# Kernel tuning notes

Measured on AMD Instinct MI355X. Metric: run time of the kernel, lower is better.

## Reference

```python
import jax, jax.numpy as jnp
import numpy as np

S_CONST = float(np.log(9.0))   # self.s = log(9)
K = 1.0                        # soft_sign sharpness (config.k)
RHO = 1.0
ALPHA0 = 0.01
BETA0 = 0.1
DECAY = 0.99


def soft_sign(x, k=K):
    # E2Efold soft sign: sigmoid(2*k*x)
    return jax.nn.sigmoid(2.0 * k * x)


def constraint_matrix(x):
    # x: [B, L, 4] -> m: [B, L, L]; pairing constraint AU+CG+UG outer products,
    # symmetrized, with |i-j|<=3 band zeroed (diags mask in torch version).
    base_a, base_u, base_c, base_g = x[..., 0], x[..., 1], x[..., 2], x[..., 3]

    def sym_outer(p, q):
        m = p[:, :, None] * q[:, None, :]
        return m + jnp.swapaxes(m, -1, -2)

    m = sym_outer(base_a, base_u) + sym_outer(base_c, base_g) + sym_outer(base_u, base_g)
    L = x.shape[1]
    i = jnp.arange(L)
    band = jnp.abs(i[:, None] - i[None, :]) <= 3  # [L, L] bool
    return jnp.where(band, jnp.zeros((), m.dtype), m)


def contact_a(a_hat, m):
    a = a_hat * a_hat
    a = (a + jnp.swapaxes(a, -1, -2)) * 0.5
    return a * m


def setup_inputs() -> dict:
    key = jax.random.key(0)
    k1, k2 = jax.random.split(key)
    B, L = 16, 512
    u = jax.random.normal(k1, (B, L, L), jnp.float32) * 2.0
    x = jax.random.uniform(k2, (B, L, 4), jnp.float32)
    return {"u": u, "x": x, "timesteps": 20}


def reference(u, x, timesteps):
    m = constraint_matrix(x)
    u = soft_sign(u - S_CONST) * u
    a_hat = jax.nn.sigmoid(u) * jax.lax.stop_gradient(soft_sign(u - S_CONST))
    a = contact_a(a_hat, m)
    lmbd = jax.lax.stop_gradient(jax.nn.relu(jnp.sum(a, -1) - 1.0))

    # per-step decayed learning rates: step t uses alpha0*decay^t (for grad step)
    # and alpha0*decay^(t+1) for the soft-threshold (torch decays alpha in between)
    t_idx = jnp.arange(timesteps, dtype=jnp.float32)
    alphas = ALPHA0 * DECAY ** t_idx
    betas = BETA0 * DECAY ** t_idx

    def step(carry, ab):
        lmbd, a, a_hat = carry
        alpha, beta = ab
        grad_a = -u / 2.0 + (lmbd * soft_sign(jnp.sum(a, -1) - 1.0))[..., None]
        grad = a_hat * m * (grad_a + jnp.swapaxes(grad_a, -1, -2))
        a_hat_new = a_hat - alpha * grad
        a_hat_new = jax.nn.relu(jnp.abs(a_hat_new) - RHO * alpha * DECAY)
        a_hat_new = jnp.clip(a_hat_new, -1.0, 1.0)
        a_new = contact_a(a_hat_new, m)
        lmbd_new = lmbd + beta * jax.nn.relu(jnp.sum(a_new, -1) - 1.0)
        return (lmbd_new, a_new, a_hat_new), a_new

    _, a_stack = jax.lax.scan(step, (lmbd, a, a_hat), (alphas, betas))
    return a_stack  # [timesteps, B, L, L] == a_t_list[1:]
```

## Files before the change

kernel.cpp:

```cpp
#include <hip/hip_runtime.h>
#include <math.h>

#define BB 16
#define LL 512
#define TS 20
#define TT 64
#define NT (LL / TT)
#define NPAIR (NT * (NT + 1) / 2)
#define NUNIT 32
#define NBLK (BB * NUNIT)
#define BLL (BB * LL * LL)
#define NROW (BB * LL)
#define RSPSTEP (BB * NT * LL)

#define S_CONST 2.19722457733621938f

typedef float float4n __attribute__((ext_vector_type(4)));

__device__ __forceinline__ float sgm(float v) { return 1.0f / (1.0f + __expf(-v)); }
__device__ __forceinline__ float ahat_of(float up) {
  return sgm(up) * sgm(2.0f * (up - S_CONST));
}

__device__ __forceinline__ void st_agent(float* p, float v) {
  __hip_atomic_store(p, v, __ATOMIC_RELAXED, __HIP_MEMORY_SCOPE_AGENT);
}
__device__ __forceinline__ float ld_agent(const float* p) {
  return __hip_atomic_load(p, __ATOMIC_RELAXED, __HIP_MEMORY_SCOPE_AGENT);
}

__device__ __forceinline__ void bar_lds() {
  asm volatile("s_waitcnt lgkmcnt(0)" ::: "memory");
  __builtin_amdgcn_s_barrier();
  asm volatile("" ::: "memory");
}

__device__ __forceinline__ void decode_unit(int p, int& RI, int& RJ, bool& dg) {
  if (p < 28) {
    int base = 0, i = 0;
    while (p >= base + (NT - 1 - i)) { base += NT - 1 - i; ++i; }
    RI = i;
    RJ = i + 1 + (p - base);
    dg = false;
  } else {
    int g = p - 28;
    RI = 2 * g;
    RJ = 2 * g + 1;
    dg = true;
  }
}

__global__ __launch_bounds__(256, 2) void k_fused(const float* __restrict__ u,
                                                  const float* __restrict__ x,
                                                  float* __restrict__ rsp,
                                                  float* __restrict__ out) {
  __shared__ float t1[TT][TT + 1];
  __shared__ float t2[TT][TT + 1];
  __shared__ float colp1[16][TT];
  __shared__ float colp2[16][TT];
  __shared__ float rp1[TT];
  __shared__ float rp2[TT];
  __shared__ float xr[2][TT][4];
  __shared__ float xt[2][TT][4];
  __shared__ float cI[TT];
  __shared__ float cJ[TT];

  int b = blockIdx.x / NUNIT;
  int p = blockIdx.x % NUNIT;
  int RI, RJ;
  bool dg;
  decode_unit(p, RI, RJ, dg);
  int C1 = dg ? RI : RJ;
  int C2 = dg ? RJ : RI;

  int tid = threadIdx.x;
  int tx = tid & 15, ty = tid >> 4;

  if (tid < 128) {
    int which = tid >> 6;
    int r = tid & 63;
    int gi = (which ? RJ : RI) * TT + r;
    const float* xp = x + ((b * LL) + gi) * 4;
    float A = xp[0], U = xp[1], C = xp[2], G = xp[3];
    xr[which][r][0] = A; xr[which][r][1] = U; xr[which][r][2] = C; xr[which][r][3] = G;
    xt[which][r][0] = U; xt[which][r][1] = A + G; xt[which][r][2] = G; xt[which][r][3] = C + U;
  }

  int lrow = 0;
  if (tid < 128) {
    int which = tid >> 6;
    int r = tid & 63;
    lrow = (which ? RJ : RI) * TT + r;
  }
  float lmbd = 0.0f;

  float av1[4][4], av2[4][4];
  float wv1[4][4], wv2[4][4];
  float mv1[4][4], mv2[4][4];

  __syncthreads();

#pragma unroll
  for (int k = 0; k < 4; ++k) {
    int r = ty + 16 * k;
    {
      int i = RI * TT + r;
      int off = (b * LL + i) * LL + C1 * TT + 4 * tx;
      float4 u4 = *reinterpret_cast<const float4*>(u + off);
      float uu[4] = {u4.x, u4.y, u4.z, u4.w};
#pragma unroll
      for (int q = 0; q < 4; ++q) {
        float up = sgm(2.0f * (uu[q] - S_CONST)) * uu[q];
        t1[r][4 * tx + q] = up;
        av1[k][q] = ahat_of(up);
      }
    }
    {
      int i = RJ * TT + r;
      int off = (b * LL + i) * LL + C2 * TT + 4 * tx;
      float4 u4 = *reinterpret_cast<const float4*>(u + off);
      float uu[4] = {u4.x, u4.y, u4.z, u4.w};
#pragma unroll
      for (int q = 0; q < 4; ++q) {
        float up = sgm(2.0f * (uu[q] - S_CONST)) * uu[q];
        t2[r][4 * tx + q] = up;
        av2[k][q] = ahat_of(up);
      }
    }
  }
  __syncthreads();

  {
    float (*T1)[TT + 1] = dg ? t1 : t2;
    float (*T2)[TT + 1] = dg ? t2 : t1;
    float (*xc1)[4] = dg ? xt[0] : xt[1];
    float (*xc2)[4] = dg ? xt[1] : xt[0];
    float* rsp0 = rsp;

#pragma unroll
    for (int k = 0; k < 4; ++k) {
      int r = ty + 16 * k;
      {
        int i = RI * TT + r;
        float rs = 0.0f;
#pragma unroll
        for (int q = 0; q < 4; ++q) {
          int c = 4 * tx + q;
          int j = C1 * TT + c;
          float upT = T1[c][r];
          wv1[k][q] = -(t1[r][c] + upT);
          int d = i - j; d = d < 0 ? -d : d;
          float mm = (d <= 3) ? 0.0f
                              : xr[0][r][0] * xc1[c][0] + xr[0][r][1] * xc1[c][1] +
                                    xr[0][r][2] * xc1[c][2] + xr[0][r][3] * xc1[c][3];
          float mh = 0.5f * mm;
          mv1[k][q] = mh;
          float aT = ahat_of(upT);
          float a = av1[k][q];
          rs += (a * a + aT * aT) * mh;
        }
        rs += __shfl_xor(rs, 1); rs += __shfl_xor(rs, 2);
        rs += __shfl_xor(rs, 4); rs += __shfl_xor(rs, 8);
        if (tx == 0) st_agent(&rsp0[(b * NT + C1) * LL + i], rs + 1.0f);
      }
      {
        int i = RJ * TT + r;
        float rs = 0.0f;
#pragma unroll
        for (int q = 0; q < 4; ++q) {
          int c = 4 * tx + q;
          int j = C2 * TT + c;
          float upT = T2[c][r];
          wv2[k][q] = -(t2[r][c] + upT);
          int d = i - j; d = d < 0 ? -d : d;
          float mm = (d <= 3) ? 0.0f
                              : xr[1][r][0] * xc2[c][0] + xr[1][r][1] * xc2[c][1] +
                                    xr[1][r][2] * xc2[c][2] + xr[1][r][3] * xc2[c][3];
          float mh = 0.5f * mm;
          mv2[k][q] = mh;
          float aT = ahat_of(upT);
          float a = av2[k][q];
          rs += (a * a + aT * aT) * mh;
        }
        rs += __shfl_xor(rs, 1); rs += __shfl_xor(rs, 2);
        rs += __shfl_xor(rs, 4); rs += __shfl_xor(rs, 8);
        if (tx == 0) st_agent(&rsp0[(b * NT + C2) * LL + i], rs + 1.0f);
      }
    }
  }

  float (*T1)[TT + 1] = dg ? t1 : t2;
  float (*T2)[TT + 1] = dg ? t2 : t1;

  float alpha = 0.01f;
  float beta_prev = 0.0f;

  for (int t = 0; t < TS; ++t) {
    if (tid < 128) {
      const float* rp = rsp + (size_t)t * RSPSTEP + b * NT * LL + lrow;
      float v0, v1, v2, v3, v4, v5, v6, v7;
      for (;;) {
        v0 = ld_agent(rp + 0 * LL);
        v1 = ld_agent(rp + 1 * LL);
        v2 = ld_agent(rp + 2 * LL);
        v3 = ld_agent(rp + 3 * LL);
        v4 = ld_agent(rp + 4 * LL);
        v5 = ld_agent(rp + 5 * LL);
        v6 = ld_agent(rp + 6 * LL);
        v7 = ld_agent(rp + 7 * LL);
        bool ok = (v0 != 0.0f) & (v1 != 0.0f) & (v2 != 0.0f) & (v3 != 0.0f) &
                  (v4 != 0.0f) & (v5 != 0.0f) & (v6 != 0.0f) & (v7 != 0.0f);
        if (__all(ok)) break;
        __builtin_amdgcn_s_sleep(2);
        asm volatile("" ::: "memory");
      }
      float rsv = ((v0 + v1) + (v2 + v3)) + ((v4 + v5) + (v6 + v7));
      float dv = rsv - 9.0f;
      float rel = dv > 0.0f ? dv : 0.0f;
      lmbd = (t == 0) ? rel : lmbd + beta_prev * rel;
      float cv2 = 2.0f * (lmbd * sgm(2.0f * dv));
      if (tid >= 64) cJ[tid & 63] = cv2; else cI[tid] = cv2;
    }
    bar_lds();

    float thr = alpha * 0.99f;
    float* cc1 = dg ? cI : cJ;
    float* cc2 = dg ? cJ : cI;

    float cq1[4], cq2[4];
#pragma unroll
    for (int q = 0; q < 4; ++q) {
      cq1[q] = cc1[4 * tx + q];
      cq2[q] = cc2[4 * tx + q];
    }

    float cp1[4] = {0.f, 0.f, 0.f, 0.f};
    float cp2[4] = {0.f, 0.f, 0.f, 0.f};
#pragma unroll
    for (int k = 0; k < 4; ++k) {
      int r = ty + 16 * k;
      {
        float ci = cI[r];
        float rsv = 0.0f;
#pragma unroll
        for (int q = 0; q < 4; ++q) {
          int c = 4 * tx + q;
          float a = av1[k][q];
          float mh = mv1[k][q];
          float s2 = wv1[k][q] + ci + cq1[q];
          float tt = mh * s2;
          float sc = fmaf(-alpha, tt, 1.0f);
          float an = a * sc;
          float f = fabsf(an) - thr;
          an = fminf(fmaxf(f, 0.0f), 1.0f);
          av1[k][q] = an;
          float v = an * an * mh;
          t1[r][c] = v;
          rsv += v;
          cp1[q] += v;
        }
        rsv += __shfl_xor(rsv, 1); rsv += __shfl_xor(rsv, 2);
        rsv += __shfl_xor(rsv, 4); rsv += __shfl_xor(rsv, 8);
        if (tx == 0) rp1[r] = rsv;
      }
      {
        float ci = cJ[r];
        float rsv = 0.0f;
#pragma unroll
        for (int q = 0; q < 4; ++q) {
          int c = 4 * tx + q;
          float a = av2[k][q];
          float mh = mv2[k][q];
          float s2 = wv2[k][q] + ci + cq2[q];
          float tt = mh * s2;
          float sc = fmaf(-alpha, tt, 1.0f);
          float an = a * sc;
          float f = fabsf(an) - thr;
          an = fminf(fmaxf(f, 0.0f), 1.0f);
          av2[k][q] = an;
          float v = an * an * mh;
          t2[r][c] = v;
          rsv += v;
          cp2[q] += v;
        }
        rsv += __shfl_xor(rsv, 1); rsv += __shfl_xor(rsv, 2);
        rsv += __shfl_xor(rsv, 4); rsv += __shfl_xor(rsv, 8);
        if (tx == 0) rp2[r] = rsv;
      }
    }
#pragma unroll
    for (int q = 0; q < 4; ++q) {
      colp1[ty][4 * tx + q] = cp1[q];
      colp2[ty][4 * tx + q] = cp2[q];
    }
    bar_lds();

    if (tid < 128) {
      if (t < TS - 1) {
        float* rs_next = rsp + (size_t)(t + 1) * RSPSTEP;
        if (tid < 64) {
          int i = tid;
          float vsum = rp1[i];
          float (*cpA)[TT] = dg ? colp1 : colp2;
#pragma unroll
          for (int y = 0; y < 16; ++y) vsum += cpA[y][i];
          st_agent(&rs_next[(b * NT + C1) * LL + RI * TT + i], vsum + 1.0f);
        } else {
          int i = tid - 64;
          float vsum = rp2[i];
          float (*cpB)[TT] = dg ? colp2 : colp1;
#pragma unroll
          for (int y = 0; y < 16; ++y) vsum += cpB[y][i];
          st_agent(&rs_next[(b * NT + C2) * LL + RJ * TT + i], vsum + 1.0f);
        }
      }
    } else {
      int tid2 = tid - 128;
      int tx2 = tid2 & 15, ty2 = tid2 >> 4;
      float* op = out + (size_t)t * BLL;
#pragma unroll
      for (int k = 0; k < 8; ++k) {
        int r = ty2 + 8 * k;
        {
          int off = (b * LL + RI * TT + r) * LL + C1 * TT + 4 * tx2;
          float4n res;
#pragma unroll
          for (int q = 0; q < 4; ++q) {
            int c = 4 * tx2 + q;
            res[q] = t1[r][c] + T1[c][r];
          }
          __builtin_nontemporal_store(res, reinterpret_cast<float4n*>(op + off));
        }
        {
          int off = (b * LL + RJ * TT + r) * LL + C2 * TT + 4 * tx2;
          float4n res;
#pragma unroll
          for (int q = 0; q < 4; ++q) {
            int c = 4 * tx2 + q;
            res[q] = t2[r][c] + T2[c][r];
          }
          __builtin_nontemporal_store(res, reinterpret_cast<float4n*>(op + off));
        }
      }
    }

    beta_prev = (t == 0) ? 0.1f : beta_prev * 0.99f;
    alpha *= 0.99f;
  }
}

__device__ __forceinline__ void decode_pair(int p, int& I, int& J) {
  int base = 0, i = 0;
  while (p >= base + (NT - i)) { base += NT - i; ++i; }
  I = i;
  J = i + (p - base);
}

__global__ __launch_bounds__(256) void k_init(const float* __restrict__ u,
                                              const float* __restrict__ x,
                                              float* __restrict__ w,
                                              float* __restrict__ ah,
                                              float* __restrict__ rowsum) {
  __shared__ float up1[TT][TT + 1];
  __shared__ float up2[TT][TT + 1];
  __shared__ float xr[2][TT][4];
  __shared__ float xt[2][TT][4];

  int b = blockIdx.x / NPAIR;
  int p = blockIdx.x % NPAIR;
  int I, J;
  decode_pair(p, I, J);
  bool diag = (I == J);
  int tid = threadIdx.x;
  int tx = tid & 15, ty = tid >> 4;

  if (tid < 128) {
    int which = tid >> 6;
    int r = tid & 63;
    int gi = (which ? J : I) * TT + r;
    const float* xp = x + ((b * LL) + gi) * 4;
    float A = xp[0], U = xp[1], C = xp[2], G = xp[3];
    xr[which][r][0] = A; xr[which][r][1] = U; xr[which][r][2] = C; xr[which][r][3] = G;
    xt[which][r][0] = U; xt[which][r][1] = A + G; xt[which][r][2] = G; xt[which][r][3] = C + U;
  }

  float a1r[4][4], a2r[4][4];

#pragma unroll
  for (int k = 0; k < 4; ++k) {
    int r = ty + 16 * k;
    {
      int i = I * TT + r;
      int off = (b * LL + i) * LL + J * TT + 4 * tx;
      float4 u4 = *reinterpret_cast<const float4*>(u + off);
      float uu[4] = {u4.x, u4.y, u4.z, u4.w};
      float av[4];
#pragma unroll
      for (int q = 0; q < 4; ++q) {
        float up = sgm(2.0f * (uu[q] - S_CONST)) * uu[q];
        up1[r][4 * tx + q] = up;
        av[q] = ahat_of(up);
        a1r[k][q] = av[q];
      }
      *reinterpret_cast<float4*>(ah + off) = make_float4(av[0], av[1], av[2], av[3]);
    }
    if (!diag) {
      int i = J * TT + r;
      int off = (b * LL + i) * LL + I * TT + 4 * tx;
      float4 u4 = *reinterpret_cast<const float4*>(u + off);
      float uu[4] = {u4.x, u4.y, u4.z, u4.w};
      float av[4];
#pragma unroll
      for (int q = 0; q < 4; ++q) {
        float up = sgm(2.0f * (uu[q] - S_CONST)) * uu[q];
        up2[r][4 * tx + q] = up;
        av[q] = ahat_of(up);
        a2r[k][q] = av[q];
      }
      *reinterpret_cast<float4*>(ah + off) = make_float4(av[0], av[1], av[2], av[3]);
    }
  }
  __syncthreads();

  float (*U2)[TT + 1] = diag ? up1 : up2;

#pragma unroll
  for (int k = 0; k < 4; ++k) {
    int r = ty + 16 * k;
    {
      int i = I * TT + r;
      int off = (b * LL + i) * LL + J * TT + 4 * tx;
      float wv[4];
      float rs = 0.0f;
#pragma unroll
      for (int q = 0; q < 4; ++q) {
        int c = 4 * tx + q;
        int j = J * TT + c;
        float upT = U2[c][r];
        wv[q] = -0.5f * (up1[r][c] + upT);
        int d = i - j; d = d < 0 ? -d : d;
        float mm = (d <= 3) ? 0.0f
                            : xr[0][r][0] * xt[1][c][0] + xr[0][r][1] * xt[1][c][1] +
                                  xr[0][r][2] * xt[1][c][2] + xr[0][r][3] * xt[1][c][3];
        float aT = ahat_of(upT);
        float a = a1r[k][q];
        rs += 0.5f * (a * a + aT * aT) * mm;
      }
      *reinterpret_cast<float4*>(w + off) = make_float4(wv[0], wv[1], wv[2], wv[3]);
      rs += __shfl_xor(rs, 1); rs += __shfl_xor(rs, 2);
      rs += __shfl_xor(rs, 4); rs += __shfl_xor(rs, 8);
      if (tx == 0) atomicAdd(&rowsum[b * LL + i], rs);
    }
    if (!diag) {
      int i = J * TT + r;
      int off = (b * LL + i) * LL + I * TT + 4 * tx;
      float wv[4];
      float rs = 0.0f;
#pragma unroll
      for (int q = 0; q < 4; ++q) {
        int c = 4 * tx + q;
        int j = I * TT + c;
        float upT = up1[c][r];
        wv[q] = -0.5f * (up2[r][c] + upT);
        int d = i - j; d = d < 0 ? -d : d;
        float mm = (d <= 3) ? 0.0f
                            : xr[1][r][0] * xt[0][c][0] + xr[1][r][1] * xt[0][c][1] +
                                  xr[1][r][2] * xt[0][c][2] + xr[1][r][3] * xt[0][c][3];
        float aT = ahat_of(upT);
        float a = a2r[k][q];
        rs += 0.5f * (a * a + aT * aT) * mm;
      }
      *reinterpret_cast<float4*>(w + off) = make_float4(wv[0], wv[1], wv[2], wv[3]);
      rs += __shfl_xor(rs, 1); rs += __shfl_xor(rs, 2);
      rs += __shfl_xor(rs, 4); rs += __shfl_xor(rs, 8);
      if (tx == 0) atomicAdd(&rowsum[b * LL + i], rs);
    }
  }
}

__global__ __launch_bounds__(256) void k_c(float* __restrict__ lmbd,
                                           const float* __restrict__ rs,
                                           float* __restrict__ cc,
                                           float* __restrict__ rsn,
                                           float beta_prev, int first) {
  int idx = blockIdx.x * blockDim.x + threadIdx.x;
  if (idx >= NROW) return;
  float t = rs[idx] - 1.0f;
  float rel = t > 0.0f ? t : 0.0f;
  float l = first ? rel : lmbd[idx] + beta_prev * rel;
  lmbd[idx] = l;
  cc[idx] = l * sgm(2.0f * t);
  rsn[idx] = 0.0f;
}

__global__ __launch_bounds__(256) void k_step(const float* __restrict__ x,
                                              const float* __restrict__ w,
                                              float* __restrict__ ah,
                                              const float* __restrict__ cvec,
                                              float* __restrict__ rsn,
                                              float* __restrict__ out,
                                              float alpha, float thr) {
  __shared__ float an1[TT][TT + 1];
  __shared__ float an2[TT][TT + 1];
  __shared__ float xr[2][TT][4];
  __shared__ float xt[2][TT][4];
  __shared__ float cI[TT];
  __shared__ float cJ[TT];

  int b = blockIdx.x / NPAIR;
  int p = blockIdx.x % NPAIR;
  int I, J;
  decode_pair(p, I, J);
  bool diag = (I == J);
  int tid = threadIdx.x;
  int tx = tid & 15, ty = tid >> 4;

  if (tid < 128) {
    int which = tid >> 6;
    int r = tid & 63;
    int gi = (which ? J : I) * TT + r;
    const float* xp = x + ((b * LL) + gi) * 4;
    float A = xp[0], U = xp[1], C = xp[2], G = xp[3];
    xr[which][r][0] = A; xr[which][r][1] = U; xr[which][r][2] = C; xr[which][r][3] = G;
    xt[which][r][0] = U; xt[which][r][1] = A + G; xt[which][r][2] = G; xt[which][r][3] = C + U;
  } else {
    int t2i = tid - 128;
    int which = t2i >> 6;
    int r = t2i & 63;
    int gi = (which ? J : I) * TT + r;
    float cv = cvec[b * LL + gi];
    if (which) cJ[r] = cv; else cI[r] = cv;
  }
  __syncthreads();

  float m1[4][4], m2[4][4];

#pragma unroll
  for (int k = 0; k < 4; ++k) {
    int r = ty + 16 * k;
    {
      int i = I * TT + r;
      int off = (b * LL + i) * LL + J * TT + 4 * tx;
      float4 a4 = *reinterpret_cast<const float4*>(ah + off);
      float4 w4 = *reinterpret_cast<const float4*>(w + off);
      float av[4] = {a4.x, a4.y, a4.z, a4.w};
      float wv[4] = {w4.x, w4.y, w4.z, w4.w};
      float ci = cI[r];
      float res[4];
#pragma unroll
      for (int q = 0; q < 4; ++q) {
        int c = 4 * tx + q;
        int j = J * TT + c;
        int d = i - j; d = d < 0 ? -d : d;
        float mm = (d <= 3) ? 0.0f
                            : xr[0][r][0] * xt[1][c][0] + xr[0][r][1] * xt[1][c][1] +
                                  xr[0][r][2] * xt[1][c][2] + xr[0][r][3] * xt[1][c][3];
        m1[k][q] = mm;
        float g = av[q] * mm * (wv[q] + ci + cJ[c]);
        float an = av[q] - alpha * g;
        an = fabsf(an) - thr;
        an = an > 0.0f ? an : 0.0f;
        an = an < 1.0f ? an : 1.0f;
        res[q] = an;
        an1[r][c] = an;
      }
      *reinterpret_cast<float4*>(ah + off) = make_float4(res[0], res[1], res[2], res[3]);
    }
    if (!diag) {
      int i = J * TT + r;
      int off = (b * LL + i) * LL + I * TT + 4 * tx;
      float4 a4 = *reinterpret_cast<const float4*>(ah + off);
      float4 w4 = *reinterpret_cast<const float4*>(w + off);
      float av[4] = {a4.x, a4.y, a4.z, a4.w};
      float wv[4] = {w4.x, w4.y, w4.z, w4.w};
      float ci = cJ[r];
      float res[4];
#pragma unroll
      for (int q = 0; q < 4; ++q) {
        int c = 4 * tx + q;
        int j = I * TT + c;
        int d = i - j; d = d < 0 ? -d : d;
        float mm = (d <= 3) ? 0.0f
                            : xr[1][r][0] * xt[0][c][0] + xr[1][r][1] * xt[0][c][1] +
                                  xr[1][r][2] * xt[0][c][2] + xr[1][r][3] * xt[0][c][3];
        m2[k][q] = mm;
        float g = av[q] * mm * (wv[q] + ci + cI[c]);
        float an = av[q] - alpha * g;
        an = fabsf(an) - thr;
        an = an > 0.0f ? an : 0.0f;
        an = an < 1.0f ? an : 1.0f;
        res[q] = an;
        an2[r][c] = an;
      }
      *reinterpret_cast<float4*>(ah + off) = make_float4(res[0], res[1], res[2], res[3]);
    }
  }
  __syncthreads();

  float (*A2)[TT + 1] = diag ? an1 : an2;

#pragma unroll
  for (int k = 0; k < 4; ++k) {
    int r = ty + 16 * k;
    {
      int i = I * TT + r;
      int off = (b * LL + i) * LL + J * TT + 4 * tx;
      float res[4];
      float rs = 0.0f;
#pragma unroll
      for (int q = 0; q < 4; ++q) {
        int c = 4 * tx + q;
        float a = an1[r][c];
        float bt = A2[c][r];
        float v = 0.5f * (a * a + bt * bt) * m1[k][q];
        res[q] = v;
        rs += v;
      }
      *reinterpret_cast<float4*>(out + off) = make_float4(res[0], res[1], res[2], res[3]);
      rs += __shfl_xor(rs, 1); rs += __shfl_xor(rs, 2);
      rs += __shfl_xor(rs, 4); rs += __shfl_xor(rs, 8);
      if (tx == 0) atomicAdd(&rsn[b * LL + i], rs);
    }
    if (!diag) {
      int i = J * TT + r;
      int off = (b * LL + i) * LL + I * TT + 4 * tx;
      float res[4];
      float rs = 0.0f;
#pragma unroll
      for (int q = 0; q < 4; ++q) {
        int c = 4 * tx + q;
        float a = an2[r][c];
        float bt = an1[c][r];
        float v = 0.5f * (a * a + bt * bt) * m2[k][q];
        res[q] = v;
        rs += v;
      }
      *reinterpret_cast<float4*>(out + off) = make_float4(res[0], res[1], res[2], res[3]);
      rs += __shfl_xor(rs, 1); rs += __shfl_xor(rs, 2);
      rs += __shfl_xor(rs, 4); rs += __shfl_xor(rs, 8);
      if (tx == 0) atomicAdd(&rsn[b * LL + i], rs);
    }
  }
}

extern "C" void kernel_launch(void* const* d_in, const int* in_sizes, int n_in,
                              void* d_out, int out_size, void* d_ws, size_t ws_size,
                              hipStream_t stream) {
  const float* u = (const float*)d_in[0];
  const float* x = (const float*)d_in[1];
  float* out = (float*)d_out;
  float* ws = (float*)d_ws;

  float* rsp = ws;
  (void)hipMemsetAsync(rsp, 0, (size_t)TS * RSPSTEP * sizeof(float), stream);

  void* args[] = {(void*)&u, (void*)&x, (void*)&rsp, (void*)&out};
  hipError_t err = hipLaunchCooperativeKernel((void*)k_fused, dim3(NBLK),
                                              dim3(256), args, 0, stream);
  if (err == hipSuccess) return;

  float* w = ws;
  float* ah = ws + (size_t)BLL;
  float* rsA = ws + 2 * (size_t)BLL;
  float* rsB = rsA + NROW;
  float* cc = rsB + NROW;
  float* lmbd = cc + NROW;

  (void)hipMemsetAsync(rsA, 0, NROW * sizeof(float), stream);

  dim3 grid(BB * NPAIR);
  dim3 block(256);
  k_init<<<grid, block, 0, stream>>>(u, x, w, ah, rsA);

  float* ra = rsA;
  float* rb = rsB;
  for (int t = 0; t < TS; ++t) {
    float alpha = 0.01f * powf(0.99f, (float)t);
    float beta_prev = (t > 0) ? 0.1f * powf(0.99f, (float)(t - 1)) : 0.0f;
    k_c<<<dim3((NROW + 255) / 256), block, 0, stream>>>(lmbd, ra, cc, rb, beta_prev,
                                                        t == 0 ? 1 : 0);
    k_step<<<grid, block, 0, stream>>>(x, w, ah, cc, rb, out + (size_t)t * BLL, alpha,
                                       alpha * 0.99f);
    float* tmp = ra; ra = rb; rb = tmp;
  }
}
```

Measured before the change: 398.6 us.

## Add row-panel cooperative kernel holding full rows and transpose in registers

```diff
diff --git a/kernel.cpp b/kernel.cpp
--- a/kernel.cpp
+++ b/kernel.cpp
@@ -4,6 +4,18 @@
 #define BB 16
 #define LL 512
 #define TS 20
+
+#define NPANEL 16
+#define PROWS 32
+#define NBLK2 (BB * NPANEL)
+#define CROWS (BB * LL)
+#define UTST 36
+#define UTFLOATS (512 * UTST)
+#define W2ST 516
+#define W2FLOATS (32 * W2ST)
+#define SM2_FLOATS (UTFLOATS + W2FLOATS + 512)
+#define SM2_BYTES (SM2_FLOATS * 4)
+
 #define TT 64
 #define NT (LL / TT)
 #define NPAIR (NT * (NT + 1) / 2)
@@ -33,6 +45,157 @@
   asm volatile("s_waitcnt lgkmcnt(0)" ::: "memory");
   __builtin_amdgcn_s_barrier();
   asm volatile("" ::: "memory");
+}
+
+__global__ __launch_bounds__(256, 1) void k_panel(const float* __restrict__ u,
+                                                  const float* __restrict__ x,
+                                                  float* __restrict__ cbuf,
+                                                  float* __restrict__ out) {
+  extern __shared__ float smem[];
+  float* ut = smem;
+  float* w2sh = smem + UTFLOATS;
+  float* carr = smem + UTFLOATS + W2FLOATS;
+
+  int b = blockIdx.x / NPANEL;
+  int panel = blockIdx.x % NPANEL;
+  int P0 = panel * PROWS;
+
+  int tid = threadIdx.x;
+  int tx = tid & 7;
+  int ty = tid >> 3;
+  int gi = P0 + ty;
+
+  float av[16][4], avT[16][4], mh[16][4];
+
+  {
+    int j1 = tid, j2 = tid + 256;
+    const float* xp1 = x + ((size_t)b * LL + j1) * 4;
+    const float* xp2 = x + ((size_t)b * LL + j2) * 4;
+    float A1 = xp1[0], U1 = xp1[1], C1v = xp1[2], G1 = xp1[3];
+    float A2 = xp2[0], U2 = xp2[1], C2v = xp2[2], G2 = xp2[3];
+    w2sh[j1 * 4 + 0] = U1; w2sh[j1 * 4 + 1] = A1 + G1;
+    w2sh[j1 * 4 + 2] = G1; w2sh[j1 * 4 + 3] = C1v + U1;
+    w2sh[j2 * 4 + 0] = U2; w2sh[j2 * 4 + 1] = A2 + G2;
+    w2sh[j2 * 4 + 2] = G2; w2sh[j2 * 4 + 3] = C2v + U2;
+  }
+  float4 xr = *reinterpret_cast<const float4*>(x + ((size_t)b * LL + gi) * 4);
+  __syncthreads();
+
+#pragma unroll
+  for (int k = 0; k < 16; ++k) {
+#pragma unroll
+    for (int q = 0; q < 4; ++q) {
+      int j = k * 32 + tx * 4 + q;
+      int d = gi - j; d = d < 0 ? -d : d;
+      float4n xt4 = *reinterpret_cast<float4n*>(w2sh + j * 4);
+      float mm = xr.x * xt4[0] + xr.y * xt4[1] + xr.z * xt4[2] + xr.w * xt4[3];
+      mh[k][q] = (d <= 3) ? 0.0f : 0.5f * mm;
+    }
+  }
+  __syncthreads();
+
+#pragma unroll 4
+  for (int h = 0; h < 16; ++h) {
+    int j = ty + 32 * h;
+    float4 u4 = *reinterpret_cast<const float4*>(u + ((size_t)b * LL + j) * LL + P0 + tx * 4);
+    float uu[4] = {u4.x, u4.y, u4.z, u4.w};
+    float4n st;
+#pragma unroll
+    for (int q = 0; q < 4; ++q) st[q] = sgm(2.0f * (uu[q] - S_CONST)) * uu[q];
+    *reinterpret_cast<float4n*>(ut + j * UTST + tx * 4) = st;
+  }
+  __syncthreads();
+
+  float rs0 = 0.0f;
+#pragma unroll
+  for (int k = 0; k < 16; ++k) {
+    float4 u4 = *reinterpret_cast<const float4*>(u + ((size_t)b * LL + gi) * LL + k * 32 + tx * 4);
+    float uu[4] = {u4.x, u4.y, u4.z, u4.w};
+#pragma unroll
+    for (int q = 0; q < 4; ++q) {
+      int j = k * 32 + tx * 4 + q;
+      float up = sgm(2.0f * (uu[q] - S_CONST)) * uu[q];
+      float upT = ut[j * UTST + ty];
+      w2sh[ty * W2ST + j] = -(up + upT);
+      float a0 = ahat_of(up);
+      float aT0 = ahat_of(upT);
+      av[k][q] = a0;
+      avT[k][q] = aT0;
+      rs0 += (a0 * a0 + aT0 * aT0) * mh[k][q];
+    }
+  }
+  rs0 += __shfl_xor(rs0, 1); rs0 += __shfl_xor(rs0, 2); rs0 += __shfl_xor(rs0, 4);
+  float dv0 = rs0 - 1.0f;
+  float lmbd = dv0 > 0.0f ? dv0 : 0.0f;
+  if (tx == 0) st_agent(&cbuf[(size_t)b * LL + gi], 2.0f * (lmbd * sgm(2.0f * dv0)) + 1.0f);
+
+  float alpha = 0.01f;
+  float beta = 0.1f;
+
+  for (int t = 0; t < TS; ++t) {
+    if (tid < 64) {
+      const float* cp = cbuf + (size_t)t * CROWS + (size_t)b * LL + tid;
+      float v0, v1, v2, v3, v4, v5, v6, v7;
+      for (;;) {
+        v0 = ld_agent(cp + 0 * 64); v1 = ld_agent(cp + 1 * 64);
+        v2 = ld_agent(cp + 2 * 64); v3 = ld_agent(cp + 3 * 64);
+        v4 = ld_agent(cp + 4 * 64); v5 = ld_agent(cp + 5 * 64);
+        v6 = ld_agent(cp + 6 * 64); v7 = ld_agent(cp + 7 * 64);
+        bool ok = (v0 != 0.0f) & (v1 != 0.0f) & (v2 != 0.0f) & (v3 != 0.0f) &
+                  (v4 != 0.0f) & (v5 != 0.0f) & (v6 != 0.0f) & (v7 != 0.0f);
+        if (__all(ok)) break;
+        __builtin_amdgcn_s_sleep(1);
+        asm volatile("" ::: "memory");
+      }
+      carr[tid + 0 * 64] = v0 - 1.0f; carr[tid + 1 * 64] = v1 - 1.0f;
+      carr[tid + 2 * 64] = v2 - 1.0f; carr[tid + 3 * 64] = v3 - 1.0f;
+      carr[tid + 4 * 64] = v4 - 1.0f; carr[tid + 5 * 64] = v5 - 1.0f;
+      carr[tid + 6 * 64] = v6 - 1.0f; carr[tid + 7 * 64] = v7 - 1.0f;
+    }
+    bar_lds();
+
+    float thr = alpha * 0.99f;
+    float crow = carr[gi];
+    float rsacc = 0.0f;
+    float* op = out + ((size_t)t * BB + b) * LL * LL + (size_t)gi * LL;
+#pragma unroll
+    for (int k = 0; k < 16; ++k) {
+      float4n w4 = *reinterpret_cast<float4n*>(w2sh + ty * W2ST + k * 32 + tx * 4);
+      float4n cc4 = *reinterpret_cast<float4n*>(carr + k * 32 + tx * 4);
+      float4n o4;
+#pragma unroll
+      for (int q = 0; q < 4; ++q) {
+        float m5 = mh[k][q];
+        float s = w4[q] + crow + cc4[q];
+        float F = fmaf(-alpha, m5 * s, 1.0f);
+        float an = av[k][q] * F;
+        an = fminf(fmaxf(fabsf(an) - thr, 0.0f), 1.0f);
+        float anT = avT[k][q] * F;
+        anT = fminf(fmaxf(fabsf(anT) - thr, 0.0f), 1.0f);
+        av[k][q] = an;
+        avT[k][q] = anT;
+        float o = fmaf(an, an, anT * anT) * m5;
+        o4[q] = o;
+        rsacc += o;
+      }
+      __builtin_nontemporal_store(o4, reinterpret_cast<float4n*>(op + k * 32 + tx * 4));
+    }
+
+    rsacc += __shfl_xor(rsacc, 1); rsacc += __shfl_xor(rsacc, 2); rsacc += __shfl_xor(rsacc, 4);
+    {
+      float dv = rsacc - 1.0f;
+      float rel = dv > 0.0f ? dv : 0.0f;
+      lmbd = lmbd + beta * rel;
+      if (t < TS - 1 && tx == 0) {
+        st_agent(&cbuf[(size_t)(t + 1) * CROWS + (size_t)b * LL + gi],
+                 2.0f * (lmbd * sgm(2.0f * dv)) + 1.0f);
+      }
+    }
+    bar_lds();
+
+    beta *= 0.99f;
+    alpha *= 0.99f;
+  }
 }
 
 __device__ __forceinline__ void decode_unit(int p, int& RI, int& RJ, bool& dg) {
@@ -153,11 +316,11 @@
           float mm = (d <= 3) ? 0.0f
                               : xr[0][r][0] * xc1[c][0] + xr[0][r][1] * xc1[c][1] +
                                     xr[0][r][2] * xc1[c][2] + xr[0][r][3] * xc1[c][3];
-          float mh = 0.5f * mm;
-          mv1[k][q] = mh;
+          float mhq = 0.5f * mm;
+          mv1[k][q] = mhq;
           float aT = ahat_of(upT);
           float a = av1[k][q];
-          rs += (a * a + aT * aT) * mh;
+          rs += (a * a + aT * aT) * mhq;
         }
         rs += __shfl_xor(rs, 1); rs += __shfl_xor(rs, 2);
         rs += __shfl_xor(rs, 4); rs += __shfl_xor(rs, 8);
@@ -176,11 +339,11 @@
           float mm = (d <= 3) ? 0.0f
                               : xr[1][r][0] * xc2[c][0] + xr[1][r][1] * xc2[c][1] +
                                     xr[1][r][2] * xc2[c][2] + xr[1][r][3] * xc2[c][3];
-          float mh = 0.5f * mm;
-          mv2[k][q] = mh;
+          float mhq = 0.5f * mm;
+          mv2[k][q] = mhq;
           float aT = ahat_of(upT);
           float a = av2[k][q];
-          rs += (a * a + aT * aT) * mh;
+          rs += (a * a + aT * aT) * mhq;
         }
         rs += __shfl_xor(rs, 1); rs += __shfl_xor(rs, 2);
         rs += __shfl_xor(rs, 4); rs += __shfl_xor(rs, 8);
@@ -200,14 +363,10 @@
       const float* rp = rsp + (size_t)t * RSPSTEP + b * NT * LL + lrow;
       float v0, v1, v2, v3, v4, v5, v6, v7;
       for (;;) {
-        v0 = ld_agent(rp + 0 * LL);
-        v1 = ld_agent(rp + 1 * LL);
-        v2 = ld_agent(rp + 2 * LL);
-        v3 = ld_agent(rp + 3 * LL);
-        v4 = ld_agent(rp + 4 * LL);
-        v5 = ld_agent(rp + 5 * LL);
-        v6 = ld_agent(rp + 6 * LL);
-        v7 = ld_agent(rp + 7 * LL);
+        v0 = ld_agent(rp + 0 * LL); v1 = ld_agent(rp + 1 * LL);
+        v2 = ld_agent(rp + 2 * LL); v3 = ld_agent(rp + 3 * LL);
+        v4 = ld_agent(rp + 4 * LL); v5 = ld_agent(rp + 5 * LL);
+        v6 = ld_agent(rp + 6 * LL); v7 = ld_agent(rp + 7 * LL);
         bool ok = (v0 != 0.0f) & (v1 != 0.0f) & (v2 != 0.0f) & (v3 != 0.0f) &
                   (v4 != 0.0f) & (v5 != 0.0f) & (v6 != 0.0f) & (v7 != 0.0f);
         if (__all(ok)) break;
@@ -246,15 +405,13 @@
         for (int q = 0; q < 4; ++q) {
           int c = 4 * tx + q;
           float a = av1[k][q];
-          float mh = mv1[k][q];
+          float m5 = mv1[k][q];
           float s2 = wv1[k][q] + ci + cq1[q];
-          float tt = mh * s2;
-          float sc = fmaf(-alpha, tt, 1.0f);
-          float an = a * sc;
+          float an = a * fmaf(-alpha, m5 * s2, 1.0f);
           float f = fabsf(an) - thr;
           an = fminf(fmaxf(f, 0.0f), 1.0f);
           av1[k][q] = an;
-          float v = an * an * mh;
+          float v = an * an * m5;
           t1[r][c] = v;
           rsv += v;
           cp1[q] += v;
@@ -270,15 +427,13 @@
         for (int q = 0; q < 4; ++q) {
           int c = 4 * tx + q;
           float a = av2[k][q];
-          float mh = mv2[k][q];
+          float m5 = mv2[k][q];
           float s2 = wv2[k][q] + ci + cq2[q];
-          float tt = mh * s2;
-          float sc = fmaf(-alpha, tt, 1.0f);
-          float an = a * sc;
+          float an = a * fmaf(-alpha, m5 * s2, 1.0f);
           float f = fabsf(an) - thr;
           an = fminf(fmaxf(f, 0.0f), 1.0f);
           av2[k][q] = an;
-          float v = an * an * mh;
+          float v = an * an * m5;
           t2[r][c] = v;
           rsv += v;
           cp2[q] += v;
@@ -325,20 +480,14 @@
           int off = (b * LL + RI * TT + r) * LL + C1 * TT + 4 * tx2;
           float4n res;
 #pragma unroll
-          for (int q = 0; q < 4; ++q) {
-            int c = 4 * tx2 + q;
-            res[q] = t1[r][c] + T1[c][r];
-          }
+          for (int q = 0; q < 4; ++q) res[q] = t1[r][4 * tx2 + q] + T1[4 * tx2 + q][r];
           __builtin_nontemporal_store(res, reinterpret_cast<float4n*>(op + off));
         }
         {
           int off = (b * LL + RJ * TT + r) * LL + C2 * TT + 4 * tx2;
           float4n res;
 #pragma unroll
-          for (int q = 0; q < 4; ++q) {
-            int c = 4 * tx2 + q;
-            res[q] = t2[r][c] + T2[c][r];
-          }
+          for (int q = 0; q < 4; ++q) res[q] = t2[r][4 * tx2 + q] + T2[4 * tx2 + q][r];
           __builtin_nontemporal_store(res, reinterpret_cast<float4n*>(op + off));
         }
       }
@@ -651,12 +800,24 @@
   float* out = (float*)d_out;
   float* ws = (float*)d_ws;
 
+  if (ws_size >= (size_t)(1 << 20)) {
+    hipError_t attrErr = hipFuncSetAttribute(
+        (const void*)k_panel, hipFuncAttributeMaxDynamicSharedMemorySize, SM2_BYTES);
+    if (attrErr == hipSuccess) {
+      float* cbuf = ws;
+      (void)hipMemsetAsync(cbuf, 0, (size_t)(TS + 1) * CROWS * sizeof(float), stream);
+      void* argsP[] = {(void*)&u, (void*)&x, (void*)&cbuf, (void*)&out};
+      hipError_t errP = hipLaunchCooperativeKernel((void*)k_panel, dim3(NBLK2),
+                                                   dim3(256), argsP, SM2_BYTES, stream);
+      if (errP == hipSuccess) return;
+    }
+  }
+
   float* rsp = ws;
   (void)hipMemsetAsync(rsp, 0, (size_t)TS * RSPSTEP * sizeof(float), stream);
-
   void* args[] = {(void*)&u, (void*)&x, (void*)&rsp, (void*)&out};
-  hipError_t err = hipLaunchCooperativeKernel((void*)k_fused, dim3(NBLK),
-                                              dim3(256), args, 0, stream);
+  hipError_t err = hipLaunchCooperativeKernel((void*)k_fused, dim3(NBLK), dim3(256),
+                                              args, 0, stream);
   if (err == hipSuccess) return;
 
   float* w = ws;
```

After: 396.1 us. About the same (-0.6%).
